# Optimization experiments

Hardware: AMD Instinct MI355X
Metric: run time of the kernel (lower is better)

The kernel has to match this reference:

```python
import jax, jax.numpy as jnp
import numpy as np

WS = 8
NUM_HEADS = 4
DIM = 64
H = W = 128
B = 16
EPS = 1e-5


def _rel_pos_index(ws):
    coords = np.stack(np.meshgrid(np.arange(ws), np.arange(ws), indexing='ij'))  # (2,ws,ws)
    cf = coords.reshape(2, -1)
    rel = (cf[:, :, None] - cf[:, None, :]).transpose(1, 2, 0).astype(np.int64)
    rel[..., 0] += ws - 1
    rel[..., 1] += ws - 1
    rel[..., 0] *= 2 * ws - 1
    return jnp.asarray(rel.sum(-1))  # (ws*ws, ws*ws)

_RPI = _rel_pos_index(WS)


def _ln_hw(x, g, b):
    # LayerNorm over last two dims (H,W) of (B,C,H,W), affine shape (H,W)
    mu = x.mean(axis=(-2, -1), keepdims=True)
    var = ((x - mu) ** 2).mean(axis=(-2, -1), keepdims=True)
    return (x - mu) / jnp.sqrt(var + EPS) * g + b


def _ln_c(x, g, b):
    mu = x.mean(-1, keepdims=True)
    var = ((x - mu) ** 2).mean(-1, keepdims=True)
    return (x - mu) / jnp.sqrt(var + EPS) * g + b


def _win_part(x, ws):
    # (B,C,H,W) -> (B*nW, ws*ws, C)
    b, c, hh, ww = x.shape
    x = x.reshape(b, c, hh // ws, ws, ww // ws, ws)
    return x.transpose(0, 2, 4, 3, 5, 1).reshape(b * (hh // ws) * (ww // ws), ws * ws, c)


def _win_rev(w, ws, hh, ww, b):
    # (B*nW, ws*ws, C) -> (B,C,H,W)
    c = w.shape[-1]
    w = w.reshape(b, hh // ws, ww // ws, ws, ws, c)
    return w.transpose(0, 5, 1, 3, 2, 4).reshape(b, c, hh, ww)


def _forward(x, lclg1_ln1_g, lclg1_ln1_b, lclg1_conv_w, lclg1_conv_b, lclg1_ln2_g, lclg1_ln2_b,
             lclg2_ln1_g, lclg2_ln1_b, lclg2_conv_w, lclg2_conv_b, lclg2_ln2_g, lclg2_ln2_b,
             pos1, pos2, q_w, q_b, kv_w, kv_b, rpb_table, gamma, proj_w, proj_b,
             norm2_g, norm2_b, fc1_w, fc1_b, fc2_w, fc2_b):
    b, c, hh, ww = x.shape
    h = NUM_HEADS
    hd = c // h
    n = WS * WS
    scale = hd ** -0.5

    def lclg(z, g1, b1, cw, cb, g2, b2):
        z = _ln_hw(z, g1, b1)
        z = jnp.einsum('oc,bchw->bohw', cw, z) + cb[None, :, None, None]  # 1x1 conv
        return jax.nn.gelu(_ln_hw(z, g2, b2), approximate=False)

    x1 = lclg(x, lclg1_ln1_g, lclg1_ln1_b, lclg1_conv_w, lclg1_conv_b, lclg1_ln2_g, lclg1_ln2_b)
    x2 = lclg(x, lclg2_ln1_g, lclg2_ln1_b, lclg2_conv_w, lclg2_conv_b, lclg2_ln2_g, lclg2_ln2_b)

    x1w = _win_part(x1, WS) + pos1  # (B_, N, C)
    x2w = _win_part(x2, WS) + pos2
    bw = x1w.shape[0]

    q = (x1w @ q_w.T + q_b).reshape(bw, n, h, hd).transpose(0, 2, 1, 3) * scale  # (B_,h,N,hd)
    kv = (x2w @ kv_w.T + kv_b).reshape(bw, n, 2, h, hd).transpose(2, 0, 3, 1, 4)
    k, v = kv[0], kv[1]

    attn = jnp.einsum('bhnd,bhmd->bhnm', q, k)
    bias = rpb_table[_RPI.reshape(-1)].reshape(n, n, h).transpose(2, 0, 1)  # (h,N,N)
    attn = jax.nn.softmax(attn + bias[None], axis=-1)
    o = jnp.einsum('bhnm,bhmd->bhnd', attn, v)  # (B_,h,N,hd)

    # LAM_Module: attention over head_dim channels of (B_,h,N,hd)
    y = o.transpose(0, 3, 1, 2).reshape(bw, hd, h * n)  # (B_,hd,h*N)
    energy = jnp.einsum('bik,bjk->bij', y, y)  # (B_,hd,hd)
    lam = jnp.einsum('bij,bjk->bik', jax.nn.softmax(energy, axis=-1), y)
    y = (gamma * lam + y).reshape(bw, hd, h, n).transpose(0, 2, 3, 1)  # (B_,h,N,hd)

    xo = y.transpose(0, 2, 1, 3).reshape(bw, n, c) + q.transpose(0, 2, 1, 3).reshape(bw, n, c) + x1w
    xo = xo @ proj_w.T + proj_b

    xo = _win_rev(xo, WS, hh, ww, b)  # (B,C,H,W)

    # MLP with pre-norm residual over channel dim
    t = xo.reshape(b, c, hh * ww).transpose(0, 2, 1)  # (B,HW,C)
    tn = _ln_c(t, norm2_g, norm2_b)
    t = t + (jax.nn.gelu(tn @ fc1_w.T + fc1_b, approximate=False) @ fc2_w.T + fc2_b)
    return t.transpose(0, 2, 1).reshape(b, c, hh, ww)


def setup_inputs() -> dict:
    key = jax.random.key(0)
    ks = jax.random.split(key, 16)
    d = DIM

    def rn(i, shape, sc=0.02):
        return jax.random.normal(ks[i], shape, jnp.float32) * sc

    return dict(
        x=jax.random.normal(ks[0], (B, d, H, W), jnp.float32),
        lclg1_ln1_g=jnp.ones((H, W), jnp.float32), lclg1_ln1_b=jnp.zeros((H, W), jnp.float32),
        lclg1_conv_w=rn(1, (d, d)), lclg1_conv_b=jnp.zeros((d,), jnp.float32),
        lclg1_ln2_g=jnp.ones((H, W), jnp.float32), lclg1_ln2_b=jnp.zeros((H, W), jnp.float32),
        lclg2_ln1_g=jnp.ones((H, W), jnp.float32), lclg2_ln1_b=jnp.zeros((H, W), jnp.float32),
        lclg2_conv_w=rn(2, (d, d)), lclg2_conv_b=jnp.zeros((d,), jnp.float32),
        lclg2_ln2_g=jnp.ones((H, W), jnp.float32), lclg2_ln2_b=jnp.zeros((H, W), jnp.float32),
        pos1=jnp.ones((1, WS * WS, d), jnp.float32),
        pos2=jnp.ones((1, WS * WS, d), jnp.float32),
        q_w=rn(3, (d, d)), q_b=jnp.zeros((d,), jnp.float32),
        kv_w=rn(4, (2 * d, d)), kv_b=jnp.zeros((2 * d,), jnp.float32),
        rpb_table=rn(5, ((2 * WS - 1) ** 2, NUM_HEADS)),
        gamma=jnp.full((1,), 0.1, jnp.float32),
        proj_w=rn(6, (d, d)), proj_b=jnp.zeros((d,), jnp.float32),
        norm2_g=jnp.ones((d,), jnp.float32), norm2_b=jnp.zeros((d,), jnp.float32),
        fc1_w=rn(7, (d, d)), fc1_b=jnp.zeros((d,), jnp.float32),
        fc2_w=rn(8, (d, d)), fc2_b=jnp.zeros((d,), jnp.float32),
    )


def reference(x, lclg1_ln1_g, lclg1_ln1_b, lclg1_conv_w, lclg1_conv_b, lclg1_ln2_g, lclg1_ln2_b,
              lclg2_ln1_g, lclg2_ln1_b, lclg2_conv_w, lclg2_conv_b, lclg2_ln2_g, lclg2_ln2_b,
              pos1, pos2, q_w, q_b, kv_w, kv_b, rpb_table, gamma, proj_w, proj_b,
              norm2_g, norm2_b, fc1_w, fc1_b, fc2_w, fc2_b):
    return _forward(x, lclg1_ln1_g, lclg1_ln1_b, lclg1_conv_w, lclg1_conv_b, lclg1_ln2_g, lclg1_ln2_b,
                    lclg2_ln1_g, lclg2_ln1_b, lclg2_conv_w, lclg2_conv_b, lclg2_ln2_g, lclg2_ln2_b,
                    pos1, pos2, q_w, q_b, kv_w, kv_b, rpb_table, gamma, proj_w, proj_b,
                    norm2_g, norm2_b, fc1_w, fc1_b, fc2_w, fc2_b)
```

## Files before the change

### kernel.cpp

```cpp
#include <hip/hip_runtime.h>
#include <hip/hip_bf16.h>

typedef __hip_bfloat16 bf16;
typedef __attribute__((ext_vector_type(8))) short short8;
typedef __attribute__((ext_vector_type(4))) short short4v;
typedef __attribute__((ext_vector_type(4))) float float4v;
typedef __attribute__((ext_vector_type(2))) float float2v;

__device__ __forceinline__ short f2bs(float f){
    union { bf16 h; short s; } u; u.h = __float2bfloat16(f); return u.s;
}
__device__ __forceinline__ float bs2f(short s){
    return __uint_as_float(((unsigned)(unsigned short)s) << 16);
}
__device__ __forceinline__ float gelu_exact(float x){
    float ax = fabsf(x) * 0.70710678118654752440f;
    float t  = __builtin_amdgcn_rcpf(fmaf(0.3275911f, ax, 1.0f));
    float poly = t*fmaf(t, fmaf(t, fmaf(t, fmaf(t, 1.061405429f, -1.453152027f),
                                 1.421413741f), -0.284496736f), 0.254829592f);
    float e = __expf(-ax*ax);
    float erfp = fmaf(-poly, e, 1.0f);
    float er = copysignf(erfp, x);
    return 0.5f * x * (1.0f + er);
}
#define MFMA(a,b,c) __builtin_amdgcn_mfma_f32_16x16x32_bf16((a),(b),(c),0,0,0)

#define HW 16384
#define NPLANE 1048576
#define EPS 1e-5f
#define LS 72

#define OFF_W1   0
#define OFF_W2   4096
#define OFF_QW   8192
#define OFF_KVW  12288
#define OFF_PW   20480
#define OFF_FW1  24576
#define OFF_FW2  28672

__global__ __launch_bounds__(256) void k_pre(const float* __restrict__ x,
                                             float* __restrict__ mu,
                                             float* __restrict__ rinv,
                                             const float* __restrict__ w1, const float* __restrict__ w2,
                                             const float* __restrict__ qw, const float* __restrict__ kvw,
                                             const float* __restrict__ pw, const float* __restrict__ fw1,
                                             const float* __restrict__ fw2,
                                             short* __restrict__ wb, float* __restrict__ rowsum){
    int bi = blockIdx.x;
    int tid = threadIdx.x;
    if (bi < 1024){
        const float* p = x + (size_t)bi * HW;
        float s = 0.f, ss = 0.f;
        for (int i = tid; i < HW/4; i += 256){
            float4v v = *(const float4v*)(p + i*4);
            #pragma unroll
            for (int k = 0; k < 4; k++){ s += v[k]; ss += v[k]*v[k]; }
        }
        __shared__ float rs[256], rss[256];
        rs[tid] = s; rss[tid] = ss; __syncthreads();
        for (int st = 128; st > 0; st >>= 1){
            if (tid < st){ rs[tid] += rs[tid+st]; rss[tid] += rss[tid+st]; }
            __syncthreads();
        }
        if (tid == 0){
            float m = rs[0] * (1.f/HW);
            float v = rss[0] * (1.f/HW) - m*m;
            mu[bi] = m; rinv[bi] = rsqrtf(v + EPS);
        }
    } else if (bi < 1032){
        int wi = bi - 1024;
        const float* src = wi==0?w1: wi==1?w2: wi==2?qw: wi==3?kvw: wi==4?(kvw+4096): wi==5?pw: wi==6?fw1: fw2;
        short* dst = wb + wi*4096;
        int base = tid*16;
        short8 o8[2];
        #pragma unroll
        for (int k = 0; k < 2; k++){
            float4v v0 = *(const float4v*)(src + base + 8*k);
            float4v v1 = *(const float4v*)(src + base + 8*k + 4);
            #pragma unroll
            for (int j = 0; j < 4; j++){ o8[k][j] = f2bs(v0[j]); o8[k][4+j] = f2bs(v1[j]); }
        }
        *(short8*)&dst[base]     = o8[0];
        *(short8*)&dst[base + 8] = o8[1];
    } else {
        if (tid < 128){
            int br = tid >> 6, o = tid & 63;
            const float* W = br ? w2 : w1;
            float s = 0.f;
            for (int c = 0; c < 64; c++) s += W[o*64 + c];
            rowsum[br*64 + o] = s;
        }
    }
}

__global__ __launch_bounds__(256, 4) void k_conv(const float* __restrict__ x,
                                              const float* __restrict__ mu,
                                              const float* __restrict__ rinv,
                                              const float* __restrict__ g1a, const float* __restrict__ b1a,
                                              const float* __restrict__ cb1,
                                              const float* __restrict__ g1b, const float* __restrict__ b1b,
                                              const float* __restrict__ cb2,
                                              const short* __restrict__ wb,
                                              const float* __restrict__ rowsum,
                                              float* __restrict__ partS, float* __restrict__ partQ){
    int blk = blockIdx.x;
    int b = blk >> 6; int chunk = blk & 63;
    __shared__ __align__(16) short xn_bf[64*LS];
    const int tid = threadIdx.x;
    const int wq = tid >> 6, lane = tid & 63, qd = lane >> 4, col = lane & 15;
    const float4v zf = {0.f,0.f,0.f,0.f};
    const int p = tid & 63, cq = tid >> 6;

    float4v m4[4], r4[4];
    #pragma unroll
    for (int k = 0; k < 4; k++){
        m4[k] = *(const float4v*)(mu   + b*64 + 16*cq + 4*k);
        r4[k] = *(const float4v*)(rinv + b*64 + 16*cq + 4*k);
    }
    short8 a10 = *(const short8*)&wb[OFF_W1 + (16*wq + col)*64 + 8*qd];
    short8 a11 = *(const short8*)&wb[OFF_W1 + (16*wq + col)*64 + 32 + 8*qd];
    short8 a20 = *(const short8*)&wb[OFF_W2 + (16*wq + col)*64 + 8*qd];
    short8 a21 = *(const short8*)&wb[OFF_W2 + (16*wq + col)*64 + 32 + 8*qd];
    float cb1v[4], rs1v[4], cb2v[4], rs2v[4];
    #pragma unroll
    for (int r = 0; r < 4; r++){
        int o = 16*wq + 4*qd + r;
        cb1v[r] = cb1[o]; rs1v[r] = rowsum[o];
        cb2v[r] = cb2[o]; rs2v[r] = rowsum[64 + o];
    }
    float sa[2][4]  = {{0.f,0.f,0.f,0.f},{0.f,0.f,0.f,0.f}};
    float ssa[2][4] = {{0.f,0.f,0.f,0.f},{0.f,0.f,0.f,0.f}};

    for (int tl = 0; tl < 4; tl++){
        int hw0 = chunk*256 + tl*64;
        {
            const float* xb = x + (size_t)(b*64 + 16*cq)*HW + hw0 + p;
            short8 o8[2];
            #pragma unroll
            for (int k = 0; k < 2; k++)
                #pragma unroll
                for (int j = 0; j < 8; j++){
                    int jj = 8*k + j;
                    float v = xb[(size_t)jj*HW];
                    o8[k][j] = f2bs((v - m4[jj>>2][jj&3]) * r4[jj>>2][jj&3]);
                }
            *(short8*)&xn_bf[p*LS + 16*cq]     = o8[0];
            *(short8*)&xn_bf[p*LS + 16*cq + 8] = o8[1];
        }
        __syncthreads();
        #pragma unroll
        for (int jn = 0; jn < 4; jn++){
            short8 bx0 = *(const short8*)&xn_bf[(16*jn + col)*LS + 8*qd];
            short8 bx1 = *(const short8*)&xn_bf[(16*jn + col)*LS + 32 + 8*qd];
            int hw = hw0 + 16*jn + col;
            {
                float4v acc = zf;
                acc = MFMA(a10, bx0, acc);
                acc = MFMA(a11, bx1, acc);
                float gl = g1a[hw], bl = b1a[hw];
                #pragma unroll
                for (int r = 0; r < 4; r++){
                    float v = gl*acc[r] + bl*rs1v[r] + cb1v[r];
                    sa[0][r] += v; ssa[0][r] += v*v;
                }
            }
            {
                float4v acc = zf;
                acc = MFMA(a20, bx0, acc);
                acc = MFMA(a21, bx1, acc);
                float gl = g1b[hw], bl = b1b[hw];
                #pragma unroll
                for (int r = 0; r < 4; r++){
                    float v = gl*acc[r] + bl*rs2v[r] + cb2v[r];
                    sa[1][r] += v; ssa[1][r] += v*v;
                }
            }
        }
        __syncthreads();
    }

    #pragma unroll
    for (int br = 0; br < 2; br++)
        #pragma unroll
        for (int r = 0; r < 4; r++){
            float s = sa[br][r], ss = ssa[br][r];
            s += __shfl_xor(s, 1); ss += __shfl_xor(ss, 1);
            s += __shfl_xor(s, 2); ss += __shfl_xor(ss, 2);
            s += __shfl_xor(s, 4); ss += __shfl_xor(ss, 4);
            s += __shfl_xor(s, 8); ss += __shfl_xor(ss, 8);
            if (col == 0){
                int o = 16*wq + 4*qd + r;
                size_t pi = ((size_t)(br*16 + b)*64 + o)*64 + chunk;
                partS[pi] = s; partQ[pi] = ss;
            }
        }
}

__global__ __launch_bounds__(256) void k_fin(const float* __restrict__ partS,
                                             const float* __restrict__ partQ,
                                             float* __restrict__ mu2,
                                             float* __restrict__ rinv2){
    int row = blockIdx.x*4 + (threadIdx.x >> 6);
    int lane = threadIdx.x & 63;
    float s  = partS[(size_t)row*64 + lane];
    float ss = partQ[(size_t)row*64 + lane];
    #pragma unroll
    for (int st = 1; st < 64; st <<= 1){
        s  += __shfl_xor(s,  st);
        ss += __shfl_xor(ss, st);
    }
    if (lane == 0){
        float m = s * (1.f/HW);
        float v = ss * (1.f/HW) - m*m;
        mu2[row] = m; rinv2[row] = rsqrtf(v + EPS);
    }
}

__global__ __launch_bounds__(256, 4) void k_attn(const float* __restrict__ x, float* __restrict__ outp,
                                              const float* __restrict__ mu1, const float* __restrict__ rinv1,
                                              const float* __restrict__ rowsum,
                                              const float* __restrict__ cb1, const float* __restrict__ cb2,
                                              const float* __restrict__ g1a, const float* __restrict__ b1a,
                                              const float* __restrict__ g1b, const float* __restrict__ b1b,
                                              const float* __restrict__ mu2, const float* __restrict__ rinv2,
                                              const float* __restrict__ g2a, const float* __restrict__ b2a,
                                              const float* __restrict__ g2b, const float* __restrict__ b2b,
                                              const float* __restrict__ pos1, const float* __restrict__ pos2,
                                              const short* __restrict__ wb,
                                              const float* __restrict__ qb, const float* __restrict__ kvb,
                                              const float* __restrict__ rpb, const float* __restrict__ gammap,
                                              const float* __restrict__ pb,
                                              const float* __restrict__ n2g, const float* __restrict__ n2b,
                                              const float* __restrict__ fb1,
                                              const float* __restrict__ fb2){
    int B = blockIdx.x;
    int hy = (B & 7) | ((B >> 5) & 8);
    int wx = (((B >> 9) & 7) << 1) | ((B >> 3) & 1);
    int b  = (B >> 4) & 15;

    const short* qwb  = wb + OFF_QW;
    const short* kvwb = wb + OFF_KVW;
    const short* pwb  = wb + OFF_PW;
    const short* f1b  = wb + OFF_FW1;
    const short* f2b  = wb + OFF_FW2;

    __shared__ __align__(16) char smem[40464];
    short* bufA = (short*)smem;
    short* bufK = (short*)(smem + 9216);
    short* bufV = (short*)(smem + 18432);
    short* bufQ = (short*)(smem + 27648);
    float* rpb_lds = (float*)(smem + 36864);
    float* energyS = (float*)(smem + 36864);
    short* soft_bf = (short*)(smem + 37888);
    float* XOf  = (float*)(smem + 18432);
    short* tnb  = (short*)smem;
    short* h1b  = (short*)(smem + 9216);
    float* sumS = (float*)(smem + 36864);
    float* sqS  = (float*)(smem + 37888);
    float* muS  = (float*)(smem + 38912);
    float* rinvS= (float*)(smem + 39168);

    const int tid = threadIdx.x;
    const int wq = tid >> 6, lane = tid & 63, qd = lane >> 4, col = lane & 15;
    size_t base = (size_t)b * NPLANE;
    #define HWOF(t) ((hy*8 + ((t)>>3))*128 + wx*8 + ((t)&7))

    const float4v zf = {0.f,0.f,0.f,0.f};
    const short8 zero8 = {0,0,0,0,0,0,0,0};

    for (int i = tid; i < 900; i += 256) rpb_lds[i] = rpb[i];

    {
        int t = tid & 63, cq = tid >> 6;
        int hw = HWOF(t);
        const float* mup = mu1   + b*64 + 16*cq;
        const float* rvp = rinv1 + b*64 + 16*cq;
        float4v m4[4], r4[4];
        #pragma unroll
        for (int k = 0; k < 4; k++){
            m4[k] = *(const float4v*)(mup + 4*k);
            r4[k] = *(const float4v*)(rvp + 4*k);
        }
        short8 o8[2];
        #pragma unroll
        for (int k = 0; k < 2; k++)
            #pragma unroll
            for (int j = 0; j < 8; j++){
                int jj = 8*k + j;
                float v = x[base + (size_t)(16*cq + jj)*HW + hw];
                o8[k][j] = f2bs((v - m4[jj>>2][jj&3]) * r4[jj>>2][jj&3]);
            }
        *(short8*)&bufV[t*LS + 16*cq]     = o8[0];
        *(short8*)&bufV[t*LS + 16*cq + 8] = o8[1];
    }
    __syncthreads();

    {
        short8 a10 = *(const short8*)&wb[OFF_W1 + (16*wq + col)*64 + 8*qd];
        short8 a11 = *(const short8*)&wb[OFF_W1 + (16*wq + col)*64 + 32 + 8*qd];
        short8 a20 = *(const short8*)&wb[OFF_W2 + (16*wq + col)*64 + 8*qd];
        short8 a21 = *(const short8*)&wb[OFF_W2 + (16*wq + col)*64 + 32 + 8*qd];
        float cb1v[4], rs1v[4], m2a[4], rv2a[4];
        float cb2v[4], rs2v[4], m2b[4], rv2b[4];
        #pragma unroll
        for (int r = 0; r < 4; r++){
            int o = 16*wq + 4*qd + r;
            cb1v[r] = cb1[o]; rs1v[r] = rowsum[o];
            m2a[r] = mu2[b*64 + o]; rv2a[r] = rinv2[b*64 + o];
            cb2v[r] = cb2[o]; rs2v[r] = rowsum[64 + o];
            m2b[r] = mu2[1024 + b*64 + o]; rv2b[r] = rinv2[1024 + b*64 + o];
        }
        #pragma unroll
        for (int jn = 0; jn < 4; jn++){
            int t = 16*jn + col; int hw = HWOF(t);
            short8 bx0 = *(const short8*)&bufV[t*LS + 8*qd];
            short8 bx1 = *(const short8*)&bufV[t*LS + 32 + 8*qd];
            {
                float4v acc = zf;
                acc = MFMA(a10, bx0, acc);
                acc = MFMA(a11, bx1, acc);
                float gl = g1a[hw], bl = b1a[hw], gg = g2a[hw], bo = b2a[hw];
                float4v p4 = *(const float4v*)(pos1 + t*64 + 16*wq + 4*qd);
                short4v pk;
                #pragma unroll
                for (int r = 0; r < 4; r++){
                    float v = gl*acc[r] + bl*rs1v[r] + cb1v[r];
                    float z = (v - m2a[r]) * rv2a[r] * gg + bo;
                    pk[r] = f2bs(gelu_exact(z) + p4[r]);
                }
                *(short4v*)&bufA[t*LS + 16*wq + 4*qd] = pk;
            }
            {
                float4v acc = zf;
                acc = MFMA(a20, bx0, acc);
                acc = MFMA(a21, bx1, acc);
                float gl = g1b[hw], bl = b1b[hw], gg = g2b[hw], bo = b2b[hw];
                float4v p4 = *(const float4v*)(pos2 + t*64 + 16*wq + 4*qd);
                short4v pk;
                #pragma unroll
                for (int r = 0; r < 4; r++){
                    float v = gl*acc[r] + bl*rs2v[r] + cb2v[r];
                    float z = (v - m2b[r]) * rv2b[r] * gg + bo;
                    pk[r] = f2bs(gelu_exact(z) + p4[r]);
                }
                *(short4v*)&bufQ[t*LS + 16*wq + 4*qd] = pk;
            }
        }
    }
    __syncthreads();

    {
        short8 ax0 = *(const short8*)&bufQ[(16*wq + col)*LS + 8*qd];
        short8 ax1 = *(const short8*)&bufQ[(16*wq + col)*LS + 32 + 8*qd];
        #pragma unroll
        for (int jn = 0; jn < 4; jn++){
            int c = 16*jn + col;
            short8 wv0 = *(const short8*)&kvwb[(64 + c)*64 + 8*qd];
            short8 wv1 = *(const short8*)&kvwb[(64 + c)*64 + 32 + 8*qd];
            float4v acc = zf;
            acc = MFMA(ax0, wv0, acc);
            acc = MFMA(ax1, wv1, acc);
            float bv = kvb[64 + c];
            short4v pk;
            #pragma unroll
            for (int r = 0; r < 4; r++) pk[r] = f2bs(acc[r] + bv);
            *(short4v*)&bufV[c*LS + 16*wq + 4*qd] = pk;
        }
        short8 a0 = *(const short8*)&kvwb[(16*wq + col)*64 + 8*qd];
        short8 a1 = *(const short8*)&kvwb[(16*wq + col)*64 + 32 + 8*qd];
        float kbr[4];
        #pragma unroll
        for (int r = 0; r < 4; r++) kbr[r] = kvb[16*wq + 4*qd + r];
        #pragma unroll
        for (int jn = 0; jn < 4; jn++){
            int t = 16*jn + col;
            short8 bx0 = *(const short8*)&bufQ[t*LS + 8*qd];
            short8 bx1 = *(const short8*)&bufQ[t*LS + 32 + 8*qd];
            float4v acc = zf;
            acc = MFMA(a0, bx0, acc);
            acc = MFMA(a1, bx1, acc);
            short4v pk;
            #pragma unroll
            for (int r = 0; r < 4; r++) pk[r] = f2bs(acc[r] + kbr[r]);
            *(short4v*)&bufK[t*LS + 16*wq + 4*qd] = pk;
        }
    }
    __syncthreads();

    {
        short8 a0 = *(const short8*)&qwb[(16*wq + col)*64 + 8*qd];
        short8 a1 = *(const short8*)&qwb[(16*wq + col)*64 + 32 + 8*qd];
        float qbr[4];
        #pragma unroll
        for (int r = 0; r < 4; r++) qbr[r] = qb[16*wq + 4*qd + r];
        #pragma unroll
        for (int jn = 0; jn < 4; jn++){
            int t = 16*jn + col;
            short8 bx0 = *(const short8*)&bufA[t*LS + 8*qd];
            short8 bx1 = *(const short8*)&bufA[t*LS + 32 + 8*qd];
            float4v acc = zf;
            acc = MFMA(a0, bx0, acc);
            acc = MFMA(a1, bx1, acc);
            short4v pk;
            #pragma unroll
            for (int r = 0; r < 4; r++) pk[r] = f2bs((acc[r] + qbr[r]) * 0.25f);
            *(short4v*)&bufQ[t*LS + 16*wq + 4*qd] = pk;
        }
    }
    short4v xreg[4];
    #pragma unroll
    for (int h = 0; h < 4; h++){
        short4v xr;
        #pragma unroll
        for (int r = 0; r < 4; r++)
            xr[r] = bufA[(16*wq + 4*qd + r)*LS + 16*h + col];
        xreg[h] = xr;
    }
    __syncthreads();

    int idx_t[4][4];
    {
        int t = 16*wq + col, ty = t >> 3, tx = t & 7;
        #pragma unroll
        for (int jn = 0; jn < 4; jn++)
            #pragma unroll
            for (int r = 0; r < 4; r++){
                int u = 16*jn + 4*qd + r;
                idx_t[jn][r] = (ty - (u>>3) + 7)*15 + (tx - (u&7) + 7);
            }
    }

    for (int h = 0; h < 4; h++){
        short8 bq = *(const short8*)&bufQ[(16*wq + col)*LS + h*16 + (qd & 1)*8];
        float pr[4][4];
        #pragma unroll
        for (int jn = 0; jn < 4; jn++){
            short8 ak = *(const short8*)&bufK[(16*jn + col)*LS + h*16 + (qd & 1)*8];
            if (qd >= 2) ak = zero8;
            float4v acc = MFMA(ak, bq, zf);
            #pragma unroll
            for (int r = 0; r < 4; r++)
                pr[jn][r] = acc[r] + rpb_lds[idx_t[jn][r]*4 + h];
        }
        float m = pr[0][0];
        #pragma unroll
        for (int jn = 0; jn < 4; jn++)
            #pragma unroll
            for (int r = 0; r < 4; r++) m = fmaxf(m, pr[jn][r]);
        m = fmaxf(m, __shfl_xor(m, 16));
        m = fmaxf(m, __shfl_xor(m, 32));
        float s = 0.f;
        #pragma unroll
        for (int jn = 0; jn < 4; jn++)
            #pragma unroll
            for (int r = 0; r < 4; r++){ pr[jn][r] = __expf(pr[jn][r] - m); s += pr[jn][r]; }
        s += __shfl_xor(s, 16);
        s += __shfl_xor(s, 32);
        float rc = 1.f / s;
        #pragma unroll
        for (int jn = 0; jn < 4; jn++){
            short4v pk;
            #pragma unroll
            for (int r = 0; r < 4; r++) pk[r] = f2bs(pr[jn][r] * rc);
            *(short4v*)&bufA[(16*wq + col)*LS + 16*jn + 4*qd] = pk;
        }
        short8 ap0 = *(const short8*)&bufA[(16*wq + col)*LS + 8*qd];
        short8 ap1 = *(const short8*)&bufA[(16*wq + col)*LS + 32 + 8*qd];
        short8 bv0 = *(const short8*)&bufV[(h*16 + col)*LS + 8*qd];
        short8 bv1 = *(const short8*)&bufV[(h*16 + col)*LS + 32 + 8*qd];
        float4v acc_o = zf;
        acc_o = MFMA(ap0, bv0, acc_o);
        acc_o = MFMA(ap1, bv1, acc_o);
        __syncthreads();
        short4v ot;
        #pragma unroll
        for (int r = 0; r < 4; r++) ot[r] = f2bs(acc_o[r]);
        *(short4v*)&bufV[(h*16 + col)*LS + 16*wq + 4*qd] = ot;
        #pragma unroll
        for (int r = 0; r < 4; r++)
            bufK[(16*wq + 4*qd + r)*LS + h*16 + col] = ot[r];
    }
    __syncthreads();

    {
        float4v acc_e = zf;
        #pragma unroll
        for (int h = 0; h < 4; h++){
            short8 f0 = *(const short8*)&bufV[(h*16 + col)*LS + 8*qd];
            short8 f1 = *(const short8*)&bufV[(h*16 + col)*LS + 32 + 8*qd];
            acc_e = MFMA(f0, f0, acc_e);
            acc_e = MFMA(f1, f1, acc_e);
        }
        if (wq == 0){
            #pragma unroll
            for (int r = 0; r < 4; r++) energyS[(4*qd + r)*16 + col] = acc_e[r];
        }
    }
    __syncthreads();
    if (tid < 16){
        int i = tid; float m = -1e30f;
        for (int j = 0; j < 16; j++) m = fmaxf(m, energyS[i*16 + j]);
        float s = 0.f; float e[16];
        for (int j = 0; j < 16; j++){ e[j] = __expf(energyS[i*16 + j] - m); s += e[j]; }
        float rc = 1.f / s;
        for (int j = 0; j < 16; j++) soft_bf[i*32 + j] = f2bs(e[j] * rc);
        for (int j = 0; j < 16; j++) soft_bf[i*32 + 16 + j] = 0;
    }
    __syncthreads();

    {
        float gam = gammap[0];
        short8 asf = *(const short8*)&soft_bf[col*32 + 8*qd];
        #pragma unroll
        for (int h = 0; h < 4; h++){
            short8 ay = *(const short8*)&bufK[(16*wq + col)*LS + 16*h + (qd & 1)*8];
            float4v acc = MFMA(ay, asf, zf);
            short4v xv = xreg[h];
            #pragma unroll
            for (int r = 0; r < 4; r++){
                int ro = (16*wq + 4*qd + r)*LS + 16*h + col;
                float ot = bs2f(bufK[ro]);
                float qv = bs2f(bufQ[ro]);
                float xo = gam*acc[r] + ot + qv + bs2f(xv[r]);
                bufK[ro] = f2bs(xo);
            }
        }
    }
    __syncthreads();

    {
        short8 a0 = *(const short8*)&pwb[(16*wq + col)*64 + 8*qd];
        short8 a1 = *(const short8*)&pwb[(16*wq + col)*64 + 32 + 8*qd];
        float pbr[4];
        #pragma unroll
        for (int r = 0; r < 4; r++) pbr[r] = pb[16*wq + 4*qd + r];
        #pragma unroll
        for (int jn = 0; jn < 4; jn++){
            int t = 16*jn + col;
            short8 bx0 = *(const short8*)&bufK[t*LS + 8*qd];
            short8 bx1 = *(const short8*)&bufK[t*LS + 32 + 8*qd];
            float4v acc = zf;
            acc = MFMA(a0, bx0, acc);
            acc = MFMA(a1, bx1, acc);
            float2v w0 = {acc[0]+pbr[0], acc[1]+pbr[1]};
            float2v w1 = {acc[2]+pbr[2], acc[3]+pbr[3]};
            *(float2v*)&XOf[t*66 + 16*wq + 4*qd]     = w0;
            *(float2v*)&XOf[t*66 + 16*wq + 4*qd + 2] = w1;
        }
    }
    __syncthreads();

    {
        int p = tid & 63, qg = tid >> 6;
        float s = 0.f, ss = 0.f;
        #pragma unroll
        for (int j = 0; j < 8; j++){
            float2v v = *(const float2v*)&XOf[p*66 + qg*16 + 2*j];
            s += v[0]+v[1]; ss += v[0]*v[0] + v[1]*v[1];
        }
        sumS[qg*64 + p] = s; sqS[qg*64 + p] = ss;
    }
    __syncthreads();
    if (tid < 64){
        float s  = sumS[tid] + sumS[64+tid] + sumS[128+tid] + sumS[192+tid];
        float ss = sqS[tid]  + sqS[64+tid]  + sqS[128+tid]  + sqS[192+tid];
        float m = s * (1.f/64.f);
        float var = ss * (1.f/64.f) - m*m;
        muS[tid] = m; rinvS[tid] = rsqrtf(var + EPS);
    }
    __syncthreads();
    {
        int p = tid & 63, qg = tid >> 6;
        float m = muS[p], rv = rinvS[p];
        short8 o8[2];
        #pragma unroll
        for (int k = 0; k < 2; k++)
            #pragma unroll
            for (int j = 0; j < 8; j++){
                int c = qg*16 + k*8 + j;
                o8[k][j] = f2bs((XOf[p*66 + c] - m) * rv * n2g[c] + n2b[c]);
            }
        *(short8*)&tnb[p*LS + qg*16]     = o8[0];
        *(short8*)&tnb[p*LS + qg*16 + 8] = o8[1];
    }
    __syncthreads();
    {
        short8 a0 = *(const short8*)&f1b[(16*wq + col)*64 + 8*qd];
        short8 a1 = *(const short8*)&f1b[(16*wq + col)*64 + 32 + 8*qd];
        float fbr[4];
        #pragma unroll
        for (int r = 0; r < 4; r++) fbr[r] = fb1[16*wq + 4*qd + r];
        #pragma unroll
        for (int jn = 0; jn < 4; jn++){
            int t = 16*jn + col;
            short8 bx0 = *(const short8*)&tnb[t*LS + 8*qd];
            short8 bx1 = *(const short8*)&tnb[t*LS + 32 + 8*qd];
            float4v acc = zf;
            acc = MFMA(a0, bx0, acc);
            acc = MFMA(a1, bx1, acc);
            short4v pk;
            #pragma unroll
            for (int r = 0; r < 4; r++) pk[r] = f2bs(gelu_exact(acc[r] + fbr[r]));
            *(short4v*)&h1b[t*LS + 16*wq + 4*qd] = pk;
        }
    }
    __syncthreads();
    {
        short8 a0 = *(const short8*)&h1b[(16*wq + col)*LS + 8*qd];
        short8 a1 = *(const short8*)&h1b[(16*wq + col)*LS + 32 + 8*qd];
        #pragma unroll
        for (int jn = 0; jn < 4; jn++){
            int c2 = 16*jn + col;
            short8 f0 = *(const short8*)&f2b[c2*64 + 8*qd];
            short8 f1 = *(const short8*)&f2b[c2*64 + 32 + 8*qd];
            float4v acc = zf;
            acc = MFMA(a0, f0, acc);
            acc = MFMA(a1, f1, acc);
            float bv = fb2[c2];
            float4v ov;
            #pragma unroll
            for (int r = 0; r < 4; r++)
                ov[r] = acc[r] + bv + XOf[(16*wq + 4*qd + r)*66 + c2];
            int t0 = 16*wq + 4*qd;
            *(float4v*)(outp + base + (size_t)c2*HW + HWOF(t0)) = ov;
        }
    }
    #undef HWOF
}

extern "C" void kernel_launch(void* const* d_in, const int* in_sizes, int n_in,
                              void* d_out, int out_size, void* d_ws, size_t ws_size,
                              hipStream_t stream){
    const float* x        = (const float*)d_in[0];
    const float* l1_g1    = (const float*)d_in[1];
    const float* l1_b1    = (const float*)d_in[2];
    const float* l1_cw    = (const float*)d_in[3];
    const float* l1_cb    = (const float*)d_in[4];
    const float* l1_g2    = (const float*)d_in[5];
    const float* l1_b2    = (const float*)d_in[6];
    const float* l2_g1    = (const float*)d_in[7];
    const float* l2_b1    = (const float*)d_in[8];
    const float* l2_cw    = (const float*)d_in[9];
    const float* l2_cb    = (const float*)d_in[10];
    const float* l2_g2    = (const float*)d_in[11];
    const float* l2_b2    = (const float*)d_in[12];
    const float* pos1     = (const float*)d_in[13];
    const float* pos2     = (const float*)d_in[14];
    const float* q_w      = (const float*)d_in[15];
    const float* q_b      = (const float*)d_in[16];
    const float* kv_w     = (const float*)d_in[17];
    const float* kv_b     = (const float*)d_in[18];
    const float* rpb      = (const float*)d_in[19];
    const float* gamma    = (const float*)d_in[20];
    const float* proj_w   = (const float*)d_in[21];
    const float* proj_b   = (const float*)d_in[22];
    const float* norm2_g  = (const float*)d_in[23];
    const float* norm2_b  = (const float*)d_in[24];
    const float* fc1_w    = (const float*)d_in[25];
    const float* fc1_b    = (const float*)d_in[26];
    const float* fc2_w    = (const float*)d_in[27];
    const float* fc2_b    = (const float*)d_in[28];

    float* out = (float*)d_out;

    float* partS = (float*)d_ws;
    float* partQ = partS + (size_t)2048*64;
    float* mu1   = partQ + (size_t)2048*64;
    float* rinv1 = mu1 + 1024;
    float* mu2   = rinv1 + 1024;
    float* rinv2 = mu2 + 2048;
    float* rowsumG = rinv2 + 2048;
    short* wbuf  = (short*)(rowsumG + 128);

    k_pre  <<<1033, 256, 0, stream>>>(x, mu1, rinv1,
                                      l1_cw, l2_cw, q_w, kv_w, proj_w, fc1_w, fc2_w,
                                      wbuf, rowsumG);
    k_conv <<<1024, 256, 0, stream>>>(x, mu1, rinv1,
                                      l1_g1, l1_b1, l1_cb,
                                      l2_g1, l2_b1, l2_cb,
                                      wbuf, rowsumG,
                                      partS, partQ);
    k_fin  <<<512, 256, 0, stream>>>(partS, partQ, mu2, rinv2);
    k_attn <<<4096, 256, 0, stream>>>(x, out, mu1, rinv1, rowsumG,
                                      l1_cb, l2_cb,
                                      l1_g1, l1_b1, l2_g1, l2_b1,
                                      mu2, rinv2,
                                      l1_g2, l1_b2, l2_g2, l2_b2,
                                      pos1, pos2, wbuf, q_b, kv_b,
                                      rpb, gamma, proj_b,
                                      norm2_g, norm2_b, fc1_b, fc2_b);
}
```

Baseline: 316.5 us.

## Swizzle LDS tiles, double k_conv grid, use erff for exact GELU

Replaces the padded LDS row stride (72) with an XOR swizzle over 64-wide rows in k_conv and k_attn. This shrinks shared memory per block and is meant to avoid bank conflicts without padding. k_conv now splits each plane into 128 chunks instead of 64, doubling the grid, and k_fin reads pairs of partials to match. The hand-written erf polynomial in gelu_exact is replaced by the library erff, which is more accurate but may cost more instructions.

```diff
diff --git a/kernel.cpp b/kernel.cpp
--- a/kernel.cpp
+++ b/kernel.cpp
@@ -14,21 +14,14 @@
     return __uint_as_float(((unsigned)(unsigned short)s) << 16);
 }
 __device__ __forceinline__ float gelu_exact(float x){
-    float ax = fabsf(x) * 0.70710678118654752440f;
-    float t  = __builtin_amdgcn_rcpf(fmaf(0.3275911f, ax, 1.0f));
-    float poly = t*fmaf(t, fmaf(t, fmaf(t, fmaf(t, 1.061405429f, -1.453152027f),
-                                 1.421413741f), -0.284496736f), 0.254829592f);
-    float e = __expf(-ax*ax);
-    float erfp = fmaf(-poly, e, 1.0f);
-    float er = copysignf(erfp, x);
-    return 0.5f * x * (1.0f + er);
+    return 0.5f * x * (1.0f + erff(x * 0.70710678118654752440f));
 }
 #define MFMA(a,b,c) __builtin_amdgcn_mfma_f32_16x16x32_bf16((a),(b),(c),0,0,0)
 
 #define HW 16384
 #define NPLANE 1048576
 #define EPS 1e-5f
-#define LS 72
+#define SWI(t,c) ((((t)<<6)) | (((((c)>>3) ^ ((t)&7)) & 7) << 3) | ((c)&7))
 
 #define OFF_W1   0
 #define OFF_W2   4096
@@ -104,8 +97,8 @@
                                               const float* __restrict__ rowsum,
                                               float* __restrict__ partS, float* __restrict__ partQ){
     int blk = blockIdx.x;
-    int b = blk >> 6; int chunk = blk & 63;
-    __shared__ __align__(16) short xn_bf[64*LS];
+    int b = blk >> 7; int chunk = blk & 127;
+    __shared__ __align__(16) short xn_bf[64*64];
     const int tid = threadIdx.x;
     const int wq = tid >> 6, lane = tid & 63, qd = lane >> 4, col = lane & 15;
     const float4v zf = {0.f,0.f,0.f,0.f};
@@ -131,8 +124,8 @@
     float sa[2][4]  = {{0.f,0.f,0.f,0.f},{0.f,0.f,0.f,0.f}};
     float ssa[2][4] = {{0.f,0.f,0.f,0.f},{0.f,0.f,0.f,0.f}};
 
-    for (int tl = 0; tl < 4; tl++){
-        int hw0 = chunk*256 + tl*64;
+    for (int tl = 0; tl < 2; tl++){
+        int hw0 = chunk*128 + tl*64;
         {
             const float* xb = x + (size_t)(b*64 + 16*cq)*HW + hw0 + p;
             short8 o8[2];
@@ -144,14 +137,14 @@
                     float v = xb[(size_t)jj*HW];
                     o8[k][j] = f2bs((v - m4[jj>>2][jj&3]) * r4[jj>>2][jj&3]);
                 }
-            *(short8*)&xn_bf[p*LS + 16*cq]     = o8[0];
-            *(short8*)&xn_bf[p*LS + 16*cq + 8] = o8[1];
+            *(short8*)&xn_bf[SWI(p, 16*cq)]     = o8[0];
+            *(short8*)&xn_bf[SWI(p, 16*cq + 8)] = o8[1];
         }
         __syncthreads();
         #pragma unroll
         for (int jn = 0; jn < 4; jn++){
-            short8 bx0 = *(const short8*)&xn_bf[(16*jn + col)*LS + 8*qd];
-            short8 bx1 = *(const short8*)&xn_bf[(16*jn + col)*LS + 32 + 8*qd];
+            short8 bx0 = *(const short8*)&xn_bf[SWI(16*jn + col, 8*qd)];
+            short8 bx1 = *(const short8*)&xn_bf[SWI(16*jn + col, 32 + 8*qd)];
             int hw = hw0 + 16*jn + col;
             {
                 float4v acc = zf;
@@ -190,7 +183,7 @@
             s += __shfl_xor(s, 8); ss += __shfl_xor(ss, 8);
             if (col == 0){
                 int o = 16*wq + 4*qd + r;
-                size_t pi = ((size_t)(br*16 + b)*64 + o)*64 + chunk;
+                size_t pi = ((size_t)(br*16 + b)*64 + o)*128 + chunk;
                 partS[pi] = s; partQ[pi] = ss;
             }
         }
@@ -202,8 +195,10 @@
                                              float* __restrict__ rinv2){
     int row = blockIdx.x*4 + (threadIdx.x >> 6);
     int lane = threadIdx.x & 63;
-    float s  = partS[(size_t)row*64 + lane];
-    float ss = partQ[(size_t)row*64 + lane];
+    float2v a = *(const float2v*)(partS + (size_t)row*128 + lane*2);
+    float2v b = *(const float2v*)(partQ + (size_t)row*128 + lane*2);
+    float s  = a[0]+a[1];
+    float ss = b[0]+b[1];
     #pragma unroll
     for (int st = 1; st < 64; st <<= 1){
         s  += __shfl_xor(s,  st);
@@ -244,21 +239,21 @@
     const short* f1b  = wb + OFF_FW1;
     const short* f2b  = wb + OFF_FW2;
 
-    __shared__ __align__(16) char smem[40464];
+    __shared__ __align__(16) char smem[36864];
     short* bufA = (short*)smem;
-    short* bufK = (short*)(smem + 9216);
-    short* bufV = (short*)(smem + 18432);
-    short* bufQ = (short*)(smem + 27648);
-    float* rpb_lds = (float*)(smem + 36864);
-    float* energyS = (float*)(smem + 36864);
-    short* soft_bf = (short*)(smem + 37888);
-    float* XOf  = (float*)(smem + 18432);
+    short* bufK = (short*)(smem + 8192);
+    short* bufV = (short*)(smem + 16384);
+    short* bufQ = (short*)(smem + 24576);
+    float* rpb_lds = (float*)(smem + 32768);
+    float* XOf  = (float*)(smem + 16384);
+    float* energyS = (float*)(smem + 33280);
+    short* soft_bf = (short*)(smem + 35840);
     short* tnb  = (short*)smem;
-    short* h1b  = (short*)(smem + 9216);
-    float* sumS = (float*)(smem + 36864);
-    float* sqS  = (float*)(smem + 37888);
-    float* muS  = (float*)(smem + 38912);
-    float* rinvS= (float*)(smem + 39168);
+    short* h1b  = (short*)(smem + 8192);
+    float* sumS = (float*)(smem + 33280);
+    float* sqS  = (float*)(smem + 34304);
+    float* muS  = (float*)(smem + 35328);
+    float* rinvS= (float*)(smem + 35584);
 
     const int tid = threadIdx.x;
     const int wq = tid >> 6, lane = tid & 63, qd = lane >> 4, col = lane & 15;
@@ -290,8 +285,8 @@
                 float v = x[base + (size_t)(16*cq + jj)*HW + hw];
                 o8[k][j] = f2bs((v - m4[jj>>2][jj&3]) * r4[jj>>2][jj&3]);
             }
-        *(short8*)&bufV[t*LS + 16*cq]     = o8[0];
-        *(short8*)&bufV[t*LS + 16*cq + 8] = o8[1];
+        *(short8*)&bufV[SWI(t, 16*cq)]     = o8[0];
+        *(short8*)&bufV[SWI(t, 16*cq + 8)] = o8[1];
     }
     __syncthreads();
 
@@ -313,8 +308,8 @@
         #pragma unroll
         for (int jn = 0; jn < 4; jn++){
             int t = 16*jn + col; int hw = HWOF(t);
-            short8 bx0 = *(const short8*)&bufV[t*LS + 8*qd];
-            short8 bx1 = *(const short8*)&bufV[t*LS + 32 + 8*qd];
+            short8 bx0 = *(const short8*)&bufV[SWI(t, 8*qd)];
+            short8 bx1 = *(const short8*)&bufV[SWI(t, 32 + 8*qd)];
             {
                 float4v acc = zf;
                 acc = MFMA(a10, bx0, acc);
@@ -328,7 +323,7 @@
                     float z = (v - m2a[r]) * rv2a[r] * gg + bo;
                     pk[r] = f2bs(gelu_exact(z) + p4[r]);
                 }
-                *(short4v*)&bufA[t*LS + 16*wq + 4*qd] = pk;
+                *(short4v*)&bufA[SWI(t, 16*wq + 4*qd)] = pk;
             }
             {
                 float4v acc = zf;
@@ -343,15 +338,15 @@
                     float z = (v - m2b[r]) * rv2b[r] * gg + bo;
                     pk[r] = f2bs(gelu_exact(z) + p4[r]);
                 }
-                *(short4v*)&bufQ[t*LS + 16*wq + 4*qd] = pk;
-            }
-        }
-    }
-    __syncthreads();
-
-    {
-        short8 ax0 = *(const short8*)&bufQ[(16*wq + col)*LS + 8*qd];
-        short8 ax1 = *(const short8*)&bufQ[(16*wq + col)*LS + 32 + 8*qd];
+                *(short4v*)&bufQ[SWI(t, 16*wq + 4*qd)] = pk;
+            }
+        }
+    }
+    __syncthreads();
+
+    {
+        short8 ax0 = *(const short8*)&bufQ[SWI(16*wq + col, 8*qd)];
+        short8 ax1 = *(const short8*)&bufQ[SWI(16*wq + col, 32 + 8*qd)];
         #pragma unroll
         for (int jn = 0; jn < 4; jn++){
             int c = 16*jn + col;
@@ -364,7 +359,7 @@
             short4v pk;
             #pragma unroll
             for (int r = 0; r < 4; r++) pk[r] = f2bs(acc[r] + bv);
-            *(short4v*)&bufV[c*LS + 16*wq + 4*qd] = pk;
+            *(short4v*)&bufV[SWI(c, 16*wq + 4*qd)] = pk;
         }
         short8 a0 = *(const short8*)&kvwb[(16*wq + col)*64 + 8*qd];
         short8 a1 = *(const short8*)&kvwb[(16*wq + col)*64 + 32 + 8*qd];
@@ -374,15 +369,15 @@
         #pragma unroll
         for (int jn = 0; jn < 4; jn++){
             int t = 16*jn + col;
-            short8 bx0 = *(const short8*)&bufQ[t*LS + 8*qd];
-            short8 bx1 = *(const short8*)&bufQ[t*LS + 32 + 8*qd];
+            short8 bx0 = *(const short8*)&bufQ[SWI(t, 8*qd)];
+            short8 bx1 = *(const short8*)&bufQ[SWI(t, 32 + 8*qd)];
             float4v acc = zf;
             acc = MFMA(a0, bx0, acc);
             acc = MFMA(a1, bx1, acc);
             short4v pk;
             #pragma unroll
             for (int r = 0; r < 4; r++) pk[r] = f2bs(acc[r] + kbr[r]);
-            *(short4v*)&bufK[t*LS + 16*wq + 4*qd] = pk;
+            *(short4v*)&bufK[SWI(t, 16*wq + 4*qd)] = pk;
         }
     }
     __syncthreads();
@@ -396,15 +391,15 @@
         #pragma unroll
         for (int jn = 0; jn < 4; jn++){
             int t = 16*jn + col;
-            short8 bx0 = *(const short8*)&bufA[t*LS + 8*qd];
-            short8 bx1 = *(const short8*)&bufA[t*LS + 32 + 8*qd];
+            short8 bx0 = *(const short8*)&bufA[SWI(t, 8*qd)];
+            short8 bx1 = *(const short8*)&bufA[SWI(t, 32 + 8*qd)];
             float4v acc = zf;
             acc = MFMA(a0, bx0, acc);
             acc = MFMA(a1, bx1, acc);
             short4v pk;
             #pragma unroll
             for (int r = 0; r < 4; r++) pk[r] = f2bs((acc[r] + qbr[r]) * 0.25f);
-            *(short4v*)&bufQ[t*LS + 16*wq + 4*qd] = pk;
+            *(short4v*)&bufQ[SWI(t, 16*wq + 4*qd)] = pk;
         }
     }
     short4v xreg[4];
@@ -413,7 +408,7 @@
         short4v xr;
         #pragma unroll
         for (int r = 0; r < 4; r++)
-            xr[r] = bufA[(16*wq + 4*qd + r)*LS + 16*h + col];
+            xr[r] = bufA[SWI(16*wq + 4*qd + r, 16*h + col)];
         xreg[h] = xr;
     }
     __syncthreads();
@@ -431,11 +426,11 @@
     }
 
     for (int h = 0; h < 4; h++){
-        short8 bq = *(const short8*)&bufQ[(16*wq + col)*LS + h*16 + (qd & 1)*8];
+        short8 bq = *(const short8*)&bufQ[SWI(16*wq + col, h*16 + (qd & 1)*8)];
         float pr[4][4];
         #pragma unroll
         for (int jn = 0; jn < 4; jn++){
-            short8 ak = *(const short8*)&bufK[(16*jn + col)*LS + h*16 + (qd & 1)*8];
+            short8 ak = *(const short8*)&bufK[SWI(16*jn + col, h*16 + (qd & 1)*8)];
             if (qd >= 2) ak = zero8;
             float4v acc = MFMA(ak, bq, zf);
             #pragma unroll
@@ -462,12 +457,12 @@
             short4v pk;
             #pragma unroll
             for (int r = 0; r < 4; r++) pk[r] = f2bs(pr[jn][r] * rc);
-            *(short4v*)&bufA[(16*wq + col)*LS + 16*jn + 4*qd] = pk;
-        }
-        short8 ap0 = *(const short8*)&bufA[(16*wq + col)*LS + 8*qd];
-        short8 ap1 = *(const short8*)&bufA[(16*wq + col)*LS + 32 + 8*qd];
-        short8 bv0 = *(const short8*)&bufV[(h*16 + col)*LS + 8*qd];
-        short8 bv1 = *(const short8*)&bufV[(h*16 + col)*LS + 32 + 8*qd];
+            *(short4v*)&bufA[SWI(16*wq + col, 16*jn + 4*qd)] = pk;
+        }
+        short8 ap0 = *(const short8*)&bufA[SWI(16*wq + col, 8*qd)];
+        short8 ap1 = *(const short8*)&bufA[SWI(16*wq + col, 32 + 8*qd)];
+        short8 bv0 = *(const short8*)&bufV[SWI(h*16 + col, 8*qd)];
+        short8 bv1 = *(const short8*)&bufV[SWI(h*16 + col, 32 + 8*qd)];
         float4v acc_o = zf;
         acc_o = MFMA(ap0, bv0, acc_o);
         acc_o = MFMA(ap1, bv1, acc_o);
@@ -475,10 +470,10 @@
         short4v ot;
         #pragma unroll
         for (int r = 0; r < 4; r++) ot[r] = f2bs(acc_o[r]);
-        *(short4v*)&bufV[(h*16 + col)*LS + 16*wq + 4*qd] = ot;
+        *(short4v*)&bufV[SWI(h*16 + col, 16*wq + 4*qd)] = ot;
         #pragma unroll
         for (int r = 0; r < 4; r++)
-            bufK[(16*wq + 4*qd + r)*LS + h*16 + col] = ot[r];
+            bufK[SWI(16*wq + 4*qd + r, h*16 + col)] = ot[r];
     }
     __syncthreads();
 
@@ -486,8 +481,8 @@
         float4v acc_e = zf;
         #pragma unroll
         for (int h = 0; h < 4; h++){
-            short8 f0 = *(const short8*)&bufV[(h*16 + col)*LS + 8*qd];
-            short8 f1 = *(const short8*)&bufV[(h*16 + col)*LS + 32 + 8*qd];
+            short8 f0 = *(const short8*)&bufV[SWI(h*16 + col, 8*qd)];
+            short8 f1 = *(const short8*)&bufV[SWI(h*16 + col, 32 + 8*qd)];
             acc_e = MFMA(f0, f0, acc_e);
             acc_e = MFMA(f1, f1, acc_e);
         }
@@ -513,12 +508,12 @@
         short8 asf = *(const short8*)&soft_bf[col*32 + 8*qd];
         #pragma unroll
         for (int h = 0; h < 4; h++){
-            short8 ay = *(const short8*)&bufK[(16*wq + col)*LS + 16*h + (qd & 1)*8];
+            short8 ay = *(const short8*)&bufK[SWI(16*wq + col, 16*h + (qd & 1)*8)];
             float4v acc = MFMA(ay, asf, zf);
             short4v xv = xreg[h];
             #pragma unroll
             for (int r = 0; r < 4; r++){
-                int ro = (16*wq + 4*qd + r)*LS + 16*h + col;
+                int ro = SWI(16*wq + 4*qd + r, 16*h + col);
                 float ot = bs2f(bufK[ro]);
                 float qv = bs2f(bufQ[ro]);
                 float xo = gam*acc[r] + ot + qv + bs2f(xv[r]);
@@ -537,8 +532,8 @@
         #pragma unroll
         for (int jn = 0; jn < 4; jn++){
             int t = 16*jn + col;
-            short8 bx0 = *(const short8*)&bufK[t*LS + 8*qd];
-            short8 bx1 = *(const short8*)&bufK[t*LS + 32 + 8*qd];
+            short8 bx0 = *(const short8*)&bufK[SWI(t, 8*qd)];
+            short8 bx1 = *(const short8*)&bufK[SWI(t, 32 + 8*qd)];
             float4v acc = zf;
             acc = MFMA(a0, bx0, acc);
             acc = MFMA(a1, bx1, acc);
@@ -580,8 +575,8 @@
                 int c = qg*16 + k*8 + j;
                 o8[k][j] = f2bs((XOf[p*66 + c] - m) * rv * n2g[c] + n2b[c]);
             }
-        *(short8*)&tnb[p*LS + qg*16]     = o8[0];
-        *(short8*)&tnb[p*LS + qg*16 + 8] = o8[1];
+        *(short8*)&tnb[SWI(p, qg*16)]     = o8[0];
+        *(short8*)&tnb[SWI(p, qg*16 + 8)] = o8[1];
     }
     __syncthreads();
     {
@@ -593,21 +588,21 @@
         #pragma unroll
         for (int jn = 0; jn < 4; jn++){
             int t = 16*jn + col;
-            short8 bx0 = *(const short8*)&tnb[t*LS + 8*qd];
-            short8 bx1 = *(const short8*)&tnb[t*LS + 32 + 8*qd];
+            short8 bx0 = *(const short8*)&tnb[SWI(t, 8*qd)];
+            short8 bx1 = *(const short8*)&tnb[SWI(t, 32 + 8*qd)];
             float4v acc = zf;
             acc = MFMA(a0, bx0, acc);
             acc = MFMA(a1, bx1, acc);
             short4v pk;
             #pragma unroll
             for (int r = 0; r < 4; r++) pk[r] = f2bs(gelu_exact(acc[r] + fbr[r]));
-            *(short4v*)&h1b[t*LS + 16*wq + 4*qd] = pk;
-        }
-    }
-    __syncthreads();
-    {
-        short8 a0 = *(const short8*)&h1b[(16*wq + col)*LS + 8*qd];
-        short8 a1 = *(const short8*)&h1b[(16*wq + col)*LS + 32 + 8*qd];
+            *(short4v*)&h1b[SWI(t, 16*wq + 4*qd)] = pk;
+        }
+    }
+    __syncthreads();
+    {
+        short8 a0 = *(const short8*)&h1b[SWI(16*wq + col, 8*qd)];
+        short8 a1 = *(const short8*)&h1b[SWI(16*wq + col, 32 + 8*qd)];
         #pragma unroll
         for (int jn = 0; jn < 4; jn++){
             int c2 = 16*jn + col;
@@ -664,8 +659,8 @@
     float* out = (float*)d_out;
 
     float* partS = (float*)d_ws;
-    float* partQ = partS + (size_t)2048*64;
-    float* mu1   = partQ + (size_t)2048*64;
+    float* partQ = partS + (size_t)2048*128;
+    float* mu1   = partQ + (size_t)2048*128;
     float* rinv1 = mu1 + 1024;
     float* mu2   = rinv1 + 1024;
     float* rinv2 = mu2 + 2048;
@@ -675,7 +670,7 @@
     k_pre  <<<1033, 256, 0, stream>>>(x, mu1, rinv1,
                                       l1_cw, l2_cw, q_w, kv_w, proj_w, fc1_w, fc2_w,
                                       wbuf, rowsumG);
-    k_conv <<<1024, 256, 0, stream>>>(x, mu1, rinv1,
+    k_conv <<<2048, 256, 0, stream>>>(x, mu1, rinv1,
                                       l1_g1, l1_b1, l1_cb,
                                       l2_g1, l2_b1, l2_cb,
                                       wbuf, rowsumG,
```

After: 337.8 us. 6.7% more time.
